# Kernel tuning notes

Measured on AMD Instinct MI355X. Metric: run time of the kernel, lower is better.

## Reference

```python
import jax, jax.numpy as jnp
import numpy as np

NEG_SLOPE = 0.2  # leaky_relu slope used by standard GAT attention


def _gat_layer(h, src, dst, W, a_src, a_dst, gru, n_nodes):
    """One gated multi-head GAT layer.
    h: [N, Din]; W: [H, Din, D]; a_src/a_dst: [H, D]; gru: None or (Wih,Whh,bih,bhh).
    Heads are merged by mean so output is [N, D].
    """
    Wh = jnp.einsum('nd,hdo->nho', h, W)                      # [N, H, D]
    es = jnp.einsum('nho,ho->nh', Wh, a_src)                  # [N, H]
    ed = jnp.einsum('nho,ho->nh', Wh, a_dst)                  # [N, H]
    e = jax.nn.leaky_relu(es[src] + ed[dst], NEG_SLOPE)       # [E, H]
    # edge softmax over each destination's in-neighborhood (segment softmax)
    m = jax.ops.segment_max(e, dst, num_segments=n_nodes)     # [N, H]
    w = jnp.exp(e - m[dst])                                   # [E, H]
    denom = jax.ops.segment_sum(w, dst, num_segments=n_nodes) # [N, H]
    alpha = w / denom[dst]                                    # [E, H]
    # gather-source / scatter-add aggregation
    agg = jax.ops.segment_sum(alpha[:, :, None] * Wh[src], dst,
                              num_segments=n_nodes)           # [N, H, D]
    out = jax.nn.elu(agg.mean(axis=1))                        # [N, D] (head-mean merge)
    if gru is not None:
        Wih, Whh, bih, bhh = gru
        gi = out @ Wih.T + bih                                # [N, 3D]
        gh = h @ Whh.T + bhh                                  # [N, 3D]
        ir, iz, in_ = jnp.split(gi, 3, axis=-1)
        hr, hz, hn = jnp.split(gh, 3, axis=-1)
        r = jax.nn.sigmoid(ir + hr)
        z = jax.nn.sigmoid(iz + hz)
        n = jnp.tanh(in_ + r * hn)
        out = (1.0 - z) * n + z * h                           # GRU-gated residual update
    return out


def setup_inputs() -> dict:
    N, E, D, H, OUT = 20000, 320000, 128, 4, 1
    key = jax.random.key(0)
    ks = jax.random.split(key, 24)
    sd = 1.0 / np.sqrt(D)
    inp = {
        'h': jax.random.normal(ks[0], (N, D), jnp.float32),
        'edge_index': jax.random.randint(ks[1], (2, E), 0, N, jnp.int64),
    }
    # GAT layers: layer1-3 have H heads, layer4 has 1 head
    heads = [H, H, H, 1]
    for i, hh in enumerate(heads, start=1):
        inp[f'W{i}'] = jax.random.normal(ks[2 + 3 * i], (hh, D, D), jnp.float32) * sd
        inp[f'as{i}'] = jax.random.normal(ks[3 + 3 * i], (hh, D), jnp.float32) * 0.1
        inp[f'ad{i}'] = jax.random.normal(ks[4 + 3 * i], (hh, D), jnp.float32) * 0.1
    # shared GRUSubLayer(hidden_dim) parameters (torch GRUCell layout)
    inp['Wih'] = jax.random.normal(ks[18], (3 * D, D), jnp.float32) * sd
    inp['Whh'] = jax.random.normal(ks[19], (3 * D, D), jnp.float32) * sd
    inp['bih'] = jnp.zeros((3 * D,), jnp.float32)
    inp['bhh'] = jnp.zeros((3 * D,), jnp.float32)
    # output head
    inp['W5'] = jax.random.normal(ks[20], (D, OUT), jnp.float32) * sd
    inp['b5'] = jnp.zeros((OUT,), jnp.float32)
    return inp


def reference(h, edge_index, W1, as1, ad1, W2, as2, ad2, W3, as3, ad3,
              W4, as4, ad4, Wih, Whh, bih, bhh, W5, b5):
    N = h.shape[0]
    src, dst = edge_index[0], edge_index[1]
    gru = (Wih, Whh, bih, bhh)
    h = _gat_layer(h, src, dst, W1, as1, ad1, None, N)   # require_gru=False
    h = _gat_layer(h, src, dst, W2, as2, ad2, gru, N)
    h = _gat_layer(h, src, dst, W3, as3, ad3, gru, N)
    h = _gat_layer(h, src, dst, W4, as4, ad4, gru, N)    # single head
    return jax.nn.sigmoid(h @ W5 + b5)                   # [N, out_dim]
```

## Files before the change

kernel.cpp:

```cpp
#include <hip/hip_runtime.h>
#include <math.h>

#define D 128

typedef __attribute__((ext_vector_type(8))) short bf16x8;
typedef __attribute__((ext_vector_type(4))) float f32x4;
typedef __attribute__((ext_vector_type(2))) float f32x2;

__device__ __forceinline__ float sigmoidf_(float x) { return 1.f / (1.f + __expf(-x)); }
__device__ __forceinline__ float bf2f(unsigned short u) { return __uint_as_float(((unsigned)u) << 16); }
__device__ __forceinline__ float u2f_lo(unsigned u) { return __uint_as_float(u << 16); }
__device__ __forceinline__ float u2f_hi(unsigned u) { return __uint_as_float(u & 0xffff0000u); }
__device__ __forceinline__ unsigned short f2b(float f) {
  unsigned u = __float_as_uint(f);
  return (unsigned short)((u + 0x7fffu + ((u >> 16) & 1u)) >> 16);
}
__device__ __forceinline__ float leaky_(float v) { return v > 0.f ? v : 0.2f * v; }

__device__ __forceinline__ void pack_post_elem(const float* __restrict__ W,
                                               unsigned short* __restrict__ Bp, int i, float scale) {
  int j = i & 7;
  int lane = (i >> 3) & 63;
  int rest = i >> 9;
  int db = rest & 7;
  int kb = rest >> 3;
  int k = kb * 32 + ((lane >> 4) << 3) + j;
  int d = db * 16 + (lane & 15);
  int h = k >> 7, kk = k & 127;
  Bp[i] = f2b(W[((size_t)h * 128 + kk) * 128 + d] * scale);
}
__device__ __forceinline__ void pack_gru_elem(const float* __restrict__ S,
                                              unsigned short* __restrict__ Bp, int i) {
  int j = i & 7;
  int lane = (i >> 3) & 63;
  int rest = i >> 9;
  int db = rest % 24;
  int kb = rest / 24;
  int k = kb * 32 + ((lane >> 4) << 3) + j;
  int col = db * 16 + (lane & 15);
  Bp[i] = f2b(S[(size_t)col * 128 + k]);
}

__global__ void __launch_bounds__(256) k_prep(const float* __restrict__ h0, unsigned short* __restrict__ h0b,
// ... 107 lines not shown
  if ((int)blockIdx.x < nS) {
    int e = blockIdx.x * 256 + threadIdx.x;
    if (e < E) {
      int pos = atomicAdd(&fill[dst[e]], 1);
      srcs[pos] = src[e];
    }
    return;
  }
  const int blk = blockIdx.x - nS;
  const int w = threadIdx.x >> 6;
  const int lane = threadIdx.x & 63;
  const int r = lane & 15, g = lane >> 4;
  const int n0 = blk * 64 + w * 16;
  f32x4 acc = (f32x4)0.f;
  const int koff = g << 3;
#pragma unroll
  for (int kb = 0; kb < 4; ++kb) {
    int row = min(n0 + r, N - 1);
    bf16x8 a = *(const bf16x8*)&hb[(size_t)row * 128 + kb * 32 + koff];
    bf16x8 b = *(const bf16x8*)&Pp[((size_t)(kb * 64) + lane) * 8];
    acc = __builtin_amdgcn_mfma_f32_16x16x32_bf16(a, b, acc, 0, 0, 0);
  }
  const int rbase = n0 + g * 4;
#pragma unroll
  for (int i = 0; i < 4; ++i) {
    int row = rbase + i;
    if (row < N) {
      if (r < 4) es[(size_t)row * 4 + r] = acc[i];
      else if (r < 8) ed[(size_t)row * 4 + (r - 4)] = acc[i];
    }
  }
}

template <int H>
__global__ void __launch_bounds__(256) k_edge_gather(const int* __restrict__ rowptr,
                                                     const int* __restrict__ srcs,
                                                     const float* __restrict__ es,
                                                     const float* __restrict__ ed,
                                                     const unsigned short* __restrict__ hb,
                                                     unsigned short* __restrict__ tb, int N) {
  __shared__ __align__(16) unsigned s_off[8][32];
  __shared__ __align__(16) float s_af[8][32][H == 1 ? 1 : 4];
  const int slot = threadIdx.x >> 5;
  const int t = blockIdx.x * 8 + slot;
  if (t >= N) return;
  const int l = threadIdx.x & 31;
  const int q = l & 15;
  const int eg = l >> 4;
  const int b0 = rowptr[t];
  const int deg = rowptr[t + 1] - b0;
  unsigned short* trow = tb + (size_t)t * (H * 128);
  if (deg == 0) {
    if (l < 16) {
#pragma unroll
      for (int h = 0; h < H; ++h)
        *(uint4*)&trow[h * 128 + q * 8] = make_uint4(0u, 0u, 0u, 0u);
    }
    return;
  }
  float edv[H];
#pragma unroll
  for (int h = 0; h < H; ++h) edv[h] = ed[(size_t)t * H + h];

  f32x2 acc[H][4];
#pragma unroll
  for (int h = 0; h < H; ++h)
#pragma unroll
    for (int j = 0; j < 4; ++j) acc[h][j] = (f32x2)0.f;
  const char* hbase = (const char*)hb + q * 16;

  if (deg <= 32) {
    const bool act = l < deg;
    int s = 0;
    float vv[H];
    if (act) {
      s = srcs[b0 + l];
      if constexpr (H == 4) {
        float4 ev = *(const float4*)&es[(size_t)s * 4];
        vv[0] = leaky_(ev.x + edv[0]);
        vv[1] = leaky_(ev.y + edv[1]);
        vv[2] = leaky_(ev.z + edv[2]);
        vv[3] = leaky_(ev.w + edv[3]);
      } else {
        vv[0] = leaky_(es[s] + edv[0]);
      }
    } else {
#pragma unroll
      for (int h = 0; h < H; ++h) vv[h] = -1e30f;
    }
    float mv[H];
#pragma unroll
    for (int h = 0; h < H; ++h) mv[h] = vv[h];
#pragma unroll
    for (int off = 16; off; off >>= 1)
#pragma unroll
      for (int h = 0; h < H; ++h) mv[h] = fmaxf(mv[h], __shfl_xor(mv[h], off));
    float e[H], den[H];
#pragma unroll
    for (int h = 0; h < H; ++h) {
      e[h] = act ? __expf(vv[h] - mv[h]) : 0.f;
      den[h] = e[h];
    }
#pragma unroll
    for (int off = 16; off; off >>= 1)
#pragma unroll
      for (int h = 0; h < H; ++h) den[h] += __shfl_xor(den[h], off);
    s_off[slot][l] = act ? ((unsigned)s << 8) : 0u;
#pragma unroll
    for (int h = 0; h < H; ++h) s_af[slot][l][h] = e[h] * (1.f / den[h]);
    const int steps = (deg + 1) >> 1;
#pragma unroll 4
    for (int e2 = 0; e2 < steps; ++e2) {
      const int ei = e2 * 2 + eg;
      unsigned off = s_off[slot][ei];
      float af[H];
      if constexpr (H == 4) {
        float4 a4 = *(const float4*)&s_af[slot][ei][0];
        af[0] = a4.x; af[1] = a4.y; af[2] = a4.z; af[3] = a4.w;
      } else {
        af[0] = s_af[slot][ei][0];
      }
      uint4 v = *(const uint4*)(hbase + off);
      f32x2 vf0 = {u2f_lo(v.x), u2f_hi(v.x)};
      f32x2 vf1 = {u2f_lo(v.y), u2f_hi(v.y)};
      f32x2 vf2 = {u2f_lo(v.z), u2f_hi(v.z)};
      f32x2 vf3 = {u2f_lo(v.w), u2f_hi(v.w)};
#pragma unroll
      for (int h = 0; h < H; ++h) {
        f32x2 a2 = {af[h], af[h]};
        acc[h][0] += a2 * vf0;
        acc[h][1] += a2 * vf1;
        acc[h][2] += a2 * vf2;
        acc[h][3] += a2 * vf3;
      }
    }
  } else {
    float m[H], den[H], vreg[H];
    int sreg = 0;
#pragma unroll
    for (int h = 0; h < H; ++h) {
      m[h] = -1e30f;
      den[h] = 0.f;
      vreg[h] = -1e30f;
    }
    for (int i = l; i < deg; i += 32) {
      int s = srcs[b0 + i];
      float vv[H];
      if constexpr (H == 4) {
        float4 ev = *(const float4*)&es[(size_t)s * 4];
        vv[0] = ev.x + edv[0];
        vv[1] = ev.y + edv[1];
        vv[2] = ev.z + edv[2];
        vv[3] = ev.w + edv[3];
      } else {
        vv[0] = es[s] + edv[0];
      }
#pragma unroll
      for (int h = 0; h < H; ++h) {
        float v = leaky_(vv[h]);
        vv[h] = v;
        float nm = fmaxf(m[h], v);
        den[h] = den[h] * __expf(m[h] - nm) + __expf(v - nm);
        m[h] = nm;
      }
      if (i == l) {
        sreg = s;
#pragma unroll
        for (int h = 0; h < H; ++h) vreg[h] = vv[h];
      }
    }
#pragma unroll
    for (int off = 16; off; off >>= 1) {
#pragma unroll
      for (int h = 0; h < H; ++h) {
        float om = __shfl_xor(m[h], off);
        float od = __shfl_xor(den[h], off);
        float nm = fmaxf(m[h], om);
        den[h] = den[h] * __expf(m[h] - nm) + od * __expf(om - nm);
        m[h] = nm;
      }
    }
    float rden[H];
#pragma unroll
    for (int h = 0; h < H; ++h) rden[h] = 1.f / den[h];
    for (int c0 = 0; c0 < deg; c0 += 32) {
      const int ce = min(32, deg - c0);
      if (c0 == 0) {
        bool ok = l < deg;
        s_off[slot][l] = ok ? ((unsigned)sreg << 8) : 0u;
#pragma unroll
        for (int h = 0; h < H; ++h)
          s_af[slot][l][h] = ok ? (__expf(vreg[h] - m[h]) * rden[h]) : 0.f;
      } else {
        int i = c0 + l;
        bool ok = i < deg;
        int s = ok ? srcs[b0 + i] : 0;
        s_off[slot][l] = ok ? ((unsigned)s << 8) : 0u;
        float af[H];
#pragma unroll
        for (int h = 0; h < H; ++h) af[h] = 0.f;
        if (ok) {
          float vv[H];
          if constexpr (H == 4) {
            float4 ev = *(const float4*)&es[(size_t)s * 4];
            vv[0] = ev.x + edv[0];
            vv[1] = ev.y + edv[1];
            vv[2] = ev.z + edv[2];
            vv[3] = ev.w + edv[3];
          } else {
            vv[0] = es[s] + edv[0];
          }
#pragma unroll
          for (int h = 0; h < H; ++h)
            af[h] = __expf(leaky_(vv[h]) - m[h]) * rden[h];
        }
#pragma unroll
        for (int h = 0; h < H; ++h) s_af[slot][l][h] = af[h];
      }
      const int steps = (ce + 1) >> 1;
#pragma unroll 4
      for (int e2 = 0; e2 < steps; ++e2) {
        const int ei = e2 * 2 + eg;
        unsigned off = s_off[slot][ei];
        float af[H];
        if constexpr (H == 4) {
          float4 a4 = *(const float4*)&s_af[slot][ei][0];
          af[0] = a4.x; af[1] = a4.y; af[2] = a4.z; af[3] = a4.w;
        } else {
          af[0] = s_af[slot][ei][0];
        }
        uint4 v = *(const uint4*)(hbase + off);
        f32x2 vf0 = {u2f_lo(v.x), u2f_hi(v.x)};
        f32x2 vf1 = {u2f_lo(v.y), u2f_hi(v.y)};
        f32x2 vf2 = {u2f_lo(v.z), u2f_hi(v.z)};
        f32x2 vf3 = {u2f_lo(v.w), u2f_hi(v.w)};
#pragma unroll
        for (int h = 0; h < H; ++h) {
          f32x2 a2 = {af[h], af[h]};
          acc[h][0] += a2 * vf0;
          acc[h][1] += a2 * vf1;
          acc[h][2] += a2 * vf2;
          acc[h][3] += a2 * vf3;
        }
      }
    }
  }
#pragma unroll
  for (int h = 0; h < H; ++h)
#pragma unroll
    for (int j = 0; j < 4; ++j) {
      acc[h][j].x += __shfl_xor(acc[h][j].x, 16);
      acc[h][j].y += __shfl_xor(acc[h][j].y, 16);
    }
  if (l < 16) {
#pragma unroll
    for (int h = 0; h < H; ++h) {
      uint4 pk;
      pk.x = (unsigned)f2b(acc[h][0].x) | ((unsigned)f2b(acc[h][0].y) << 16);
      pk.y = (unsigned)f2b(acc[h][1].x) | ((unsigned)f2b(acc[h][1].y) << 16);
      pk.z = (unsigned)f2b(acc[h][2].x) | ((unsigned)f2b(acc[h][2].y) << 16);
      pk.w = (unsigned)f2b(acc[h][3].x) | ((unsigned)f2b(acc[h][3].y) << 16);
      *(uint4*)&trow[h * 128 + q * 8] = pk;
    }
  }
}

__global__ void __launch_bounds__(256) k_post1(const unsigned short* __restrict__ tb,
                                               const unsigned short* __restrict__ Bp,
                                               float* __restrict__ houtf,
                                               unsigned short* __restrict__ houtb,
                                               const float* __restrict__ Pf,
                                               float* __restrict__ es, float* __restrict__ ed) {
  __shared__ float s_pr[16][8][4];
  const int n0 = blockIdx.x * 16;
  const int w = threadIdx.x >> 6;
  const int lane = threadIdx.x & 63;
  const int r = lane & 15, g = lane >> 4;
  f32x4 acc[2];
  acc[0] = (f32x4)0.f;
  acc[1] = (f32x4)0.f;
  const int koff = g << 3;
#pragma unroll
  for (int kb = 0; kb < 16; ++kb) {
    bf16x8 a = *(const bf16x8*)&tb[(size_t)(n0 + r) * 512 + kb * 32 + koff];
#pragma unroll
    for (int t = 0; t < 2; ++t) {
      bf16x8 b = *(const bf16x8*)&Bp[((size_t)(kb * 8 + w * 2 + t) * 64 + lane) * 8];
      acc[t] = __builtin_amdgcn_mfma_f32_16x16x32_bf16(a, b, acc[t], 0, 0, 0);
    }
  }
  float ps[4][8];
#pragma unroll
  for (int i = 0; i < 4; ++i)
#pragma unroll
    for (int c = 0; c < 8; ++c) ps[i][c] = 0.f;
#pragma unroll
  for (int t = 0; t < 2; ++t) {
    const int col = (w * 2 + t) * 16 + r;
    float4 pj0 = *(const float4*)&Pf[col * 8];
    float4 pj1 = *(const float4*)&Pf[col * 8 + 4];
#pragma unroll
    for (int i = 0; i < 4; ++i) {
      const int row = n0 + g * 4 + i;
      float o = acc[t][i];
      o = o > 0.f ? o : expm1f(o);
      houtf[(size_t)row * 128 + col] = o;
      houtb[(size_t)row * 128 + col] = f2b(o);
      ps[i][0] += o * pj0.x; ps[i][1] += o * pj0.y;
      ps[i][2] += o * pj0.z; ps[i][3] += o * pj0.w;
      ps[i][4] += o * pj1.x; ps[i][5] += o * pj1.y;
      ps[i][6] += o * pj1.z; ps[i][7] += o * pj1.w;
    }
  }
#pragma unroll
  for (int off = 1; off < 16; off <<= 1)
#pragma unroll
    for (int i = 0; i < 4; ++i)
#pragma unroll
      for (int c = 0; c < 8; ++c) ps[i][c] += __shfl_xor(ps[i][c], off);
  if (r == 0) {
#pragma unroll
    for (int i = 0; i < 4; ++i)
#pragma unroll
      for (int c = 0; c < 8; ++c) s_pr[g * 4 + i][c][w] = ps[i][c];
  }
  __syncthreads();
  if (threadIdx.x < 128) {
    int row = threadIdx.x >> 3;
    int c = threadIdx.x & 7;
    float val = s_pr[row][c][0] + s_pr[row][c][1] + s_pr[row][c][2] + s_pr[row][c][3];
    int gr = n0 + row;
    if (c < 4) es[(size_t)gr * 4 + c] = val;
    else ed[(size_t)gr * 4 + (c - 4)] = val;
  }
}

template <int KD, int MODE>
__global__ void __launch_bounds__(256) k_postgru(const unsigned short* __restrict__ tb,
                                                 const unsigned short* __restrict__ Bp,
                                                 const unsigned short* __restrict__ hb,
                                                 const float* __restrict__ hf,
                                                 const unsigned short* __restrict__ Bih,
                                                 const unsigned short* __restrict__ Bhh,
                                                 const float* __restrict__ bih,
                                                 const float* __restrict__ bhh,
                                                 float* __restrict__ houtf,
                                                 unsigned short* __restrict__ houtb,
                                                 const float* __restrict__ Pf,
                                                 float* __restrict__ es, float* __restrict__ ed, int Hn,
                                                 const float* __restrict__ W5,
                                                 const float* __restrict__ b5,
                                                 float* __restrict__ out) {
  __shared__ unsigned short xs[16][136];
  __shared__ float s_pr[16][8][4];
  const int n0 = blockIdx.x * 16;
  const int w = threadIdx.x >> 6;
  const int lane = threadIdx.x & 63;
  const int r = lane & 15, g = lane >> 4;
  const int koff = g << 3;
  {
    f32x4 acc[2];
    acc[0] = (f32x4)0.f;
    acc[1] = (f32x4)0.f;
#pragma unroll
    for (int kb = 0; kb < KD / 32; ++kb) {
      bf16x8 a = *(const bf16x8*)&tb[(size_t)(n0 + r) * KD + kb * 32 + koff];
#pragma unroll
      for (int t = 0; t < 2; ++t) {
        bf16x8 b = *(const bf16x8*)&Bp[((size_t)(kb * 8 + w * 2 + t) * 64 + lane) * 8];
        acc[t] = __builtin_amdgcn_mfma_f32_16x16x32_bf16(a, b, acc[t], 0, 0, 0);
      }
    }
#pragma unroll
    for (int t = 0; t < 2; ++t) {
      const int col = (w * 2 + t) * 16 + r;
#pragma unroll
      for (int i = 0; i < 4; ++i) {
        float o = acc[t][i];
        o = o > 0.f ? o : expm1f(o);
        xs[g * 4 + i][col] = f2b(o);
      }
    }
  }
  __syncthreads();
  const int qbase = w * 2;
  f32x4 ai[3][2], ah[3][2];
#pragma unroll
  for (int p = 0; p < 3; ++p)
#pragma unroll
    for (int t = 0; t < 2; ++t) {
      ai[p][t] = (f32x4)0.f;
      ah[p][t] = (f32x4)0.f;
    }
#pragma unroll
  for (int kb = 0; kb < 4; ++kb) {
    bf16x8 ax = *(const bf16x8*)&xs[r][kb * 32 + koff];
    bf16x8 ahr = *(const bf16x8*)&hb[(size_t)(n0 + r) * 128 + kb * 32 + koff];
#pragma unroll
    for (int p = 0; p < 3; ++p) {
#pragma unroll
      for (int t = 0; t < 2; ++t) {
        const int ct = p * 8 + qbase + t;
        bf16x8 bi = *(const bf16x8*)&Bih[((size_t)(kb * 24 + ct) * 64 + lane) * 8];
        bf16x8 bh = *(const bf16x8*)&Bhh[((size_t)(kb * 24 + ct) * 64 + lane) * 8];
        ai[p][t] = __builtin_amdgcn_mfma_f32_16x16x32_bf16(ax, bi, ai[p][t], 0, 0, 0);
        ah[p][t] = __builtin_amdgcn_mfma_f32_16x16x32_bf16(ahr, bh, ah[p][t], 0, 0, 0);
      }
    }
  }
  if constexpr (MODE == 0) {
    float ps[4][8];
#pragma unroll
    for (int i = 0; i < 4; ++i)
#pragma unroll
      for (int c = 0; c < 8; ++c) ps[i][c] = 0.f;
#pragma unroll
    for (int t = 0; t < 2; ++t) {
      const int j = (qbase + t) * 16 + r;
      const float bir = bih[j], biz = bih[128 + j], bin = bih[256 + j];
      const float bhr = bhh[j], bhz = bhh[128 + j], bhn = bhh[256 + j];
      float4 pj0 = *(const float4*)&Pf[j * 8];
      float4 pj1 = *(const float4*)&Pf[j * 8 + 4];
#pragma unroll
      for (int i = 0; i < 4; ++i) {
        const int row = n0 + g * 4 + i;
        float rr = sigmoidf_(ai[0][t][i] + bir + ah[0][t][i] + bhr);
        float z = sigmoidf_(ai[1][t][i] + biz + ah[1][t][i] + bhz);
        float nn = tanhf(ai[2][t][i] + bin + rr * (ah[2][t][i] + bhn));
        float hp = hf[(size_t)row * 128 + j];
        float o = (1.f - z) * nn + z * hp;
        houtf[(size_t)row * 128 + j] = o;
        houtb[(size_t)row * 128 + j] = f2b(o);
        ps[i][0] += o * pj0.x; ps[i][1] += o * pj0.y;
        ps[i][2] += o * pj0.z; ps[i][3] += o * pj0.w;
        ps[i][4] += o * pj1.x; ps[i][5] += o * pj1.y;
        ps[i][6] += o * pj1.z; ps[i][7] += o * pj1.w;
      }
    }
#pragma unroll
    for (int off = 1; off < 16; off <<= 1)
#pragma unroll
      for (int i = 0; i < 4; ++i)
#pragma unroll
        for (int c = 0; c < 8; ++c) ps[i][c] += __shfl_xor(ps[i][c], off);
    if (r == 0) {
#pragma unroll
      for (int i = 0; i < 4; ++i)
#pragma unroll
        for (int c = 0; c < 8; ++c) s_pr[g * 4 + i][c][w] = ps[i][c];
    }
    __syncthreads();
    if (threadIdx.x < 128) {
      int row = threadIdx.x >> 3;
      int c = threadIdx.x & 7;
      float val = s_pr[row][c][0] + s_pr[row][c][1] + s_pr[row][c][2] + s_pr[row][c][3];
      int gr = n0 + row;
      if (c < Hn) es[(size_t)gr * Hn + c] = val;
      else if (c >= 4 && c < 4 + Hn) ed[(size_t)gr * Hn + (c - 4)] = val;
    }
  } else {
    float pfin[4] = {0.f, 0.f, 0.f, 0.f};
#pragma unroll
    for (int t = 0; t < 2; ++t) {
      const int j = (qbase + t) * 16 + r;
      const float bir = bih[j], biz = bih[128 + j], bin = bih[256 + j];
      const float bhr = bhh[j], bhz = bhh[128 + j], bhn = bhh[256 + j];
      const float w5 = W5[j];
#pragma unroll
      for (int i = 0; i < 4; ++i) {
        const int row = n0 + g * 4 + i;
        float rr = sigmoidf_(ai[0][t][i] + bir + ah[0][t][i] + bhr);
        float z = sigmoidf_(ai[1][t][i] + biz + ah[1][t][i] + bhz);
        float nn = tanhf(ai[2][t][i] + bin + rr * (ah[2][t][i] + bhn));
        float hp = hf[(size_t)row * 128 + j];
        float o = (1.f - z) * nn + z * hp;
        pfin[i] += o * w5;
      }
    }
#pragma unroll
    for (int off = 1; off < 16; off <<= 1)
#pragma unroll
      for (int i = 0; i < 4; ++i) pfin[i] += __shfl_xor(pfin[i], off);
    if (r == 0) {
#pragma unroll
      for (int i = 0; i < 4; ++i) s_pr[g * 4 + i][0][w] = pfin[i];
    }
    __syncthreads();
    if (threadIdx.x < 16) {
      float s = s_pr[threadIdx.x][0][0] + s_pr[threadIdx.x][0][1] +
                s_pr[threadIdx.x][0][2] + s_pr[threadIdx.x][0][3] + b5[0];
      out[n0 + threadIdx.x] = sigmoidf_(s);
    }
  }
}

extern "C" void kernel_launch(void* const* d_in, const int* in_sizes, int n_in,
                              void* d_out, int out_size, void* d_ws, size_t ws_size,
                              hipStream_t stream) {
  const float* h0 = (const float*)d_in[0];
  const int* ei = (const int*)d_in[1];
  const float* W1 = (const float*)d_in[2];
  const float* as1 = (const float*)d_in[3];
  const float* ad1 = (const float*)d_in[4];
  const float* W2 = (const float*)d_in[5];
  const float* as2 = (const float*)d_in[6];
  const float* ad2 = (const float*)d_in[7];
  const float* W3 = (const float*)d_in[8];
  const float* as3 = (const float*)d_in[9];
  const float* ad3 = (const float*)d_in[10];
  const float* W4 = (const float*)d_in[11];
  const float* as4 = (const float*)d_in[12];
  const float* ad4 = (const float*)d_in[13];
  const float* Wih = (const float*)d_in[14];
  const float* Whh = (const float*)d_in[15];
  const float* bih = (const float*)d_in[16];
  const float* bhh = (const float*)d_in[17];
  const float* W5 = (const float*)d_in[18];
  const float* b5 = (const float*)d_in[19];

  const int N = in_sizes[0] / D;
  const int E = in_sizes[1] / 2;
  const int* src = ei;
  const int* dst = ei + E;

  float* ws = (float*)d_ws;
  unsigned short* tb = (unsigned short*)ws;
  float* hA = ws + (size_t)N * 256;
  float* hB = hA + (size_t)N * 128;
  float* es = hB + (size_t)N * 128;
  float* ed = es + (size_t)N * 4;
  unsigned short* h0b = (unsigned short*)(ed + (size_t)N * 4);
  unsigned short* hAb = h0b + (size_t)N * 128;
  unsigned short* hBb = hAb + (size_t)N * 128;
  unsigned short* B1 = hBb + (size_t)N * 128;
  unsigned short* B2 = B1 + 65536;
  unsigned short* B3 = B2 + 65536;
  unsigned short* B4 = B3 + 65536;
  unsigned short* Bih = B4 + 16384;
  unsigned short* Bhh = Bih + 49152;
  unsigned short* Pp1 = Bhh + 49152;
  float* Pf2 = (float*)(Pp1 + 2048);
  float* Pf3 = Pf2 + 1024;
  float* Pf4 = Pf3 + 1024;
  int* deg = (int*)(Pf4 + 1024);
  int* rowptr = deg + N;
  int* fill = rowptr + N + 1;
  int* srcs = fill + N;

  hipMemsetAsync(deg, 0, (size_t)N * 4, stream);
  {
    const int total = N * 128 + 311296 + 2048 + 3072 + E;
    k_prep<<<(total + 255) / 256, 256, 0, stream>>>(
        h0, h0b, W1, W2, W3, W4, Wih, Whh, B1, B2, B3, B4, Bih, Bhh,
        as1, ad1, as2, ad2, as3, ad3, as4, ad4, Pp1, Pf2, Pf3, Pf4, dst, deg, N, E);
  }
  k_scan<<<1, 1024, 0, stream>>>(deg, rowptr, fill, N);
  {
    const int nS = (E + 255) / 256;
    const int nE = (N + 63) / 64;
    k_scatter_esed<<<nS + nE, 256, 0, stream>>>(src, dst, fill, srcs, E,
                                                h0b, Pp1, es, ed, N, nS);
  }

  const int gE = (N + 7) / 8;
  const int gP = N / 16;

  k_edge_gather<4><<<gE, 256, 0, stream>>>(rowptr, srcs, es, ed, h0b, tb, N);
  k_post1<<<gP, 256, 0, stream>>>(tb, B1, hA, hAb, Pf2, es, ed);
  k_edge_gather<4><<<gE, 256, 0, stream>>>(rowptr, srcs, es, ed, hAb, tb, N);
  k_postgru<512, 0><<<gP, 256, 0, stream>>>(tb, B2, hAb, hA, Bih, Bhh, bih, bhh, hB, hBb,
                                            Pf3, es, ed, 4, nullptr, nullptr, nullptr);
  k_edge_gather<4><<<gE, 256, 0, stream>>>(rowptr, srcs, es, ed, hBb, tb, N);
  k_postgru<512, 0><<<gP, 256, 0, stream>>>(tb, B3, hBb, hB, Bih, Bhh, bih, bhh, hA, hAb,
                                            Pf4, es, ed, 1, nullptr, nullptr, nullptr);
  k_edge_gather<1><<<gE, 256, 0, stream>>>(rowptr, srcs, es, ed, hAb, tb, N);
  k_postgru<128, 1><<<gP, 256, 0, stream>>>(tb, B4, hAb, hA, Bih, Bhh, bih, bhh,
                                            nullptr, nullptr, nullptr, nullptr, nullptr, 0,
                                            W5, b5, (float*)d_out);
}
```

Baseline: 267.0 us.

## Fuse edge gather with post-projection/GRU into one kernel per layer

Merges the per-layer edge softmax/gather kernel and the following projection+GRU kernel into a single 512-thread kernel that keeps the aggregated 16-row tile in shared memory instead of writing it to a global bf16 buffer. It also double-buffers the es/ed attention logits so one layer's writes do not race with reads by other blocks of the same launch. This removes the global round-trip of the aggregation buffer and halves the launch count, at the cost of much larger shared memory per block (lower occupancy) and serialising the gather and MFMA phases within a block.

```diff
diff --git a/kernel.cpp b/kernel.cpp
--- a/kernel.cpp
+++ b/kernel.cpp
@@ -8,7 +8,6 @@
 typedef __attribute__((ext_vector_type(2))) float f32x2;
 
 __device__ __forceinline__ float sigmoidf_(float x) { return 1.f / (1.f + __expf(-x)); }
-__device__ __forceinline__ float bf2f(unsigned short u) { return __uint_as_float(((unsigned)u) << 16); }
 __device__ __forceinline__ float u2f_lo(unsigned u) { return __uint_as_float(u << 16); }
 __device__ __forceinline__ float u2f_hi(unsigned u) { return __uint_as_float(u & 0xffff0000u); }
 __device__ __forceinline__ unsigned short f2b(float f) {
@@ -182,174 +181,136 @@
   }
 }
 
-template <int H>
-__global__ void __launch_bounds__(256) k_edge_gather(const int* __restrict__ rowptr,
-                                                     const int* __restrict__ srcs,
-                                                     const float* __restrict__ es,
-                                                     const float* __restrict__ ed,
-                                                     const unsigned short* __restrict__ hb,
-                                                     unsigned short* __restrict__ tb, int N) {
-  __shared__ __align__(16) unsigned s_off[8][32];
-  __shared__ __align__(16) float s_af[8][32][H == 1 ? 1 : 4];
-  const int slot = threadIdx.x >> 5;
-  const int t = blockIdx.x * 8 + slot;
-  if (t >= N) return;
-  const int l = threadIdx.x & 31;
-  const int q = l & 15;
-  const int eg = l >> 4;
-  const int b0 = rowptr[t];
-  const int deg = rowptr[t + 1] - b0;
-  unsigned short* trow = tb + (size_t)t * (H * 128);
-  if (deg == 0) {
-    if (l < 16) {
+template <int H, int MODE>
+__global__ void __launch_bounds__(512) k_layer(const int* __restrict__ rowptr,
+                                               const int* __restrict__ srcs,
+                                               const float* __restrict__ es,
+                                               const float* __restrict__ ed,
+                                               const unsigned short* __restrict__ hbG,
+                                               const unsigned short* __restrict__ Bp,
+                                               const float* __restrict__ hf,
+                                               const unsigned short* __restrict__ Bih,
+                                               const unsigned short* __restrict__ Bhh,
+                                               const float* __restrict__ bih,
+                                               const float* __restrict__ bhh,
+                                               float* __restrict__ houtf,
+                                               unsigned short* __restrict__ houtb,
+                                               const float* __restrict__ Pf,
+                                               float* __restrict__ eso, float* __restrict__ edo, int Hn,
+                                               const float* __restrict__ W5,
+                                               const float* __restrict__ b5,
+                                               float* __restrict__ out) {
+  constexpr int KD = H * 128;
+  __shared__ unsigned short ts[16][KD + 8];
+  __shared__ unsigned short xs[16][136];
+  __shared__ float s_pr[16][8][8];
+  __shared__ __align__(16) unsigned s_off[16][32];
+  __shared__ __align__(16) float s_af[16][32][H == 1 ? 1 : 4];
+
+  const int tid = threadIdx.x;
+  const int n0 = blockIdx.x * 16;
+
+  {
+    const int slot = tid >> 5;
+    const int t = n0 + slot;
+    const int l = tid & 31;
+    const int q = l & 15;
+    const int eg = l >> 4;
+    const int b0 = rowptr[t];
+    const int deg = rowptr[t + 1] - b0;
+    if (deg == 0) {
+      if (l < 16) {
+#pragma unroll
+        for (int h = 0; h < H; ++h)
+          *(uint4*)&ts[slot][h * 128 + q * 8] = make_uint4(0u, 0u, 0u, 0u);
+      }
+    } else {
+      float edv[H];
+#pragma unroll
+      for (int h = 0; h < H; ++h) edv[h] = ed[(size_t)t * H + h];
+      f32x2 acc[H][4];
 #pragma unroll
       for (int h = 0; h < H; ++h)
-        *(uint4*)&trow[h * 128 + q * 8] = make_uint4(0u, 0u, 0u, 0u);
-    }
-    return;
-  }
-  float edv[H];
-#pragma unroll
-  for (int h = 0; h < H; ++h) edv[h] = ed[(size_t)t * H + h];
-
-  f32x2 acc[H][4];
-#pragma unroll
-  for (int h = 0; h < H; ++h)
-#pragma unroll
-    for (int j = 0; j < 4; ++j) acc[h][j] = (f32x2)0.f;
-  const char* hbase = (const char*)hb + q * 16;
-
-  if (deg <= 32) {
-    const bool act = l < deg;
-    int s = 0;
-    float vv[H];
-    if (act) {
-      s = srcs[b0 + l];
-      if constexpr (H == 4) {
-        float4 ev = *(const float4*)&es[(size_t)s * 4];
-        vv[0] = leaky_(ev.x + edv[0]);
-        vv[1] = leaky_(ev.y + edv[1]);
-        vv[2] = leaky_(ev.z + edv[2]);
-        vv[3] = leaky_(ev.w + edv[3]);
+#pragma unroll
+        for (int j = 0; j < 4; ++j) acc[h][j] = (f32x2)0.f;
+      const char* hbase = (const char*)hbG + q * 16;
+
+      if (deg <= 32) {
+        const bool act = l < deg;
+        int s = 0;
+        float vv[H];
+        if (act) {
+          s = srcs[b0 + l];
+          if constexpr (H == 4) {
+            float4 ev = *(const float4*)&es[(size_t)s * 4];
+            vv[0] = leaky_(ev.x + edv[0]);
+            vv[1] = leaky_(ev.y + edv[1]);
+            vv[2] = leaky_(ev.z + edv[2]);
+            vv[3] = leaky_(ev.w + edv[3]);
+          } else {
+            vv[0] = leaky_(es[s] + edv[0]);
+          }
+        } else {
+#pragma unroll
+          for (int h = 0; h < H; ++h) vv[h] = -1e30f;
+        }
+        float mv[H];
+#pragma unroll
+        for (int h = 0; h < H; ++h) mv[h] = vv[h];
+#pragma unroll
+        for (int off = 16; off; off >>= 1)
+#pragma unroll
+          for (int h = 0; h < H; ++h) mv[h] = fmaxf(mv[h], __shfl_xor(mv[h], off));
+        float e[H], den[H];
+#pragma unroll
+        for (int h = 0; h < H; ++h) {
+          e[h] = act ? __expf(vv[h] - mv[h]) : 0.f;
+          den[h] = e[h];
+        }
+#pragma unroll
+        for (int off = 16; off; off >>= 1)
+#pragma unroll
+          for (int h = 0; h < H; ++h) den[h] += __shfl_xor(den[h], off);
+        s_off[slot][l] = act ? ((unsigned)s << 8) : 0u;
+#pragma unroll
+        for (int h = 0; h < H; ++h) s_af[slot][l][h] = e[h] * (1.f / den[h]);
+        const int steps = (deg + 1) >> 1;
+#pragma unroll 4
+        for (int e2 = 0; e2 < steps; ++e2) {
+          const int ei = e2 * 2 + eg;
+          unsigned off = s_off[slot][ei];
+          float af[H];
+          if constexpr (H == 4) {
+            float4 a4 = *(const float4*)&s_af[slot][ei][0];
+            af[0] = a4.x; af[1] = a4.y; af[2] = a4.z; af[3] = a4.w;
+          } else {
+            af[0] = s_af[slot][ei][0];
+          }
+          uint4 v = *(const uint4*)(hbase + off);
+          f32x2 vf0 = {u2f_lo(v.x), u2f_hi(v.x)};
+          f32x2 vf1 = {u2f_lo(v.y), u2f_hi(v.y)};
+          f32x2 vf2 = {u2f_lo(v.z), u2f_hi(v.z)};
+          f32x2 vf3 = {u2f_lo(v.w), u2f_hi(v.w)};
+#pragma unroll
+          for (int h = 0; h < H; ++h) {
+            f32x2 a2 = {af[h], af[h]};
+            acc[h][0] += a2 * vf0;
+            acc[h][1] += a2 * vf1;
+            acc[h][2] += a2 * vf2;
+            acc[h][3] += a2 * vf3;
+          }
+        }
       } else {
-        vv[0] = leaky_(es[s] + edv[0]);
-      }
-    } else {
-#pragma unroll
-      for (int h = 0; h < H; ++h) vv[h] = -1e30f;
-    }
-    float mv[H];
-#pragma unroll
-    for (int h = 0; h < H; ++h) mv[h] = vv[h];
-#pragma unroll
-    for (int off = 16; off; off >>= 1)
-#pragma unroll
-      for (int h = 0; h < H; ++h) mv[h] = fmaxf(mv[h], __shfl_xor(mv[h], off));
-    float e[H], den[H];
-#pragma unroll
-    for (int h = 0; h < H; ++h) {
-      e[h] = act ? __expf(vv[h] - mv[h]) : 0.f;
-      den[h] = e[h];
-    }
-#pragma unroll
-    for (int off = 16; off; off >>= 1)
-#pragma unroll
-      for (int h = 0; h < H; ++h) den[h] += __shfl_xor(den[h], off);
-    s_off[slot][l] = act ? ((unsigned)s << 8) : 0u;
-#pragma unroll
-    for (int h = 0; h < H; ++h) s_af[slot][l][h] = e[h] * (1.f / den[h]);
-    const int steps = (deg + 1) >> 1;
-#pragma unroll 4
-    for (int e2 = 0; e2 < steps; ++e2) {
-      const int ei = e2 * 2 + eg;
-      unsigned off = s_off[slot][ei];
-      float af[H];
-      if constexpr (H == 4) {
-        float4 a4 = *(const float4*)&s_af[slot][ei][0];
-        af[0] = a4.x; af[1] = a4.y; af[2] = a4.z; af[3] = a4.w;
-      } else {
-        af[0] = s_af[slot][ei][0];
-      }
-      uint4 v = *(const uint4*)(hbase + off);
-      f32x2 vf0 = {u2f_lo(v.x), u2f_hi(v.x)};
-      f32x2 vf1 = {u2f_lo(v.y), u2f_hi(v.y)};
-      f32x2 vf2 = {u2f_lo(v.z), u2f_hi(v.z)};
-      f32x2 vf3 = {u2f_lo(v.w), u2f_hi(v.w)};
-#pragma unroll
-      for (int h = 0; h < H; ++h) {
-        f32x2 a2 = {af[h], af[h]};
-        acc[h][0] += a2 * vf0;
-        acc[h][1] += a2 * vf1;
-        acc[h][2] += a2 * vf2;
-        acc[h][3] += a2 * vf3;
-      }
-    }
-  } else {
-    float m[H], den[H], vreg[H];
-    int sreg = 0;
-#pragma unroll
-    for (int h = 0; h < H; ++h) {
-      m[h] = -1e30f;
-      den[h] = 0.f;
-      vreg[h] = -1e30f;
-    }
-    for (int i = l; i < deg; i += 32) {
-      int s = srcs[b0 + i];
-      float vv[H];
-      if constexpr (H == 4) {
-        float4 ev = *(const float4*)&es[(size_t)s * 4];
-        vv[0] = ev.x + edv[0];
-        vv[1] = ev.y + edv[1];
-        vv[2] = ev.z + edv[2];
-        vv[3] = ev.w + edv[3];
-      } else {
-        vv[0] = es[s] + edv[0];
-      }
-#pragma unroll
-      for (int h = 0; h < H; ++h) {
-        float v = leaky_(vv[h]);
-        vv[h] = v;
-        float nm = fmaxf(m[h], v);
-        den[h] = den[h] * __expf(m[h] - nm) + __expf(v - nm);
-        m[h] = nm;
-      }
-      if (i == l) {
-        sreg = s;
-#pragma unroll
-        for (int h = 0; h < H; ++h) vreg[h] = vv[h];
-      }
-    }
-#pragma unroll
-    for (int off = 16; off; off >>= 1) {
-#pragma unroll
-      for (int h = 0; h < H; ++h) {
-        float om = __shfl_xor(m[h], off);
-        float od = __shfl_xor(den[h], off);
-        float nm = fmaxf(m[h], om);
-        den[h] = den[h] * __expf(m[h] - nm) + od * __expf(om - nm);
-        m[h] = nm;
-      }
-    }
-    float rden[H];
-#pragma unroll
-    for (int h = 0; h < H; ++h) rden[h] = 1.f / den[h];
-    for (int c0 = 0; c0 < deg; c0 += 32) {
-      const int ce = min(32, deg - c0);
-      if (c0 == 0) {
-        bool ok = l < deg;
-        s_off[slot][l] = ok ? ((unsigned)sreg << 8) : 0u;
-#pragma unroll
-        for (int h = 0; h < H; ++h)
-          s_af[slot][l][h] = ok ? (__expf(vreg[h] - m[h]) * rden[h]) : 0.f;
-      } else {
-        int i = c0 + l;
-        bool ok = i < deg;
-        int s = ok ? srcs[b0 + i] : 0;
-        s_off[slot][l] = ok ? ((unsigned)s << 8) : 0u;
-        float af[H];
-#pragma unroll
-        for (int h = 0; h < H; ++h) af[h] = 0.f;
-        if (ok) {
+        float m[H], den[H], vreg[H];
+        int sreg = 0;
+#pragma unroll
+        for (int h = 0; h < H; ++h) {
+          m[h] = -1e30f;
+          den[h] = 0.f;
+          vreg[h] = -1e30f;
+        }
+        for (int i = l; i < deg; i += 32) {
+          int s = srcs[b0 + i];
           float vv[H];
           if constexpr (H == 4) {
             float4 ev = *(const float4*)&es[(size_t)s * 4];
@@ -361,98 +322,142 @@
             vv[0] = es[s] + edv[0];
           }
 #pragma unroll
-          for (int h = 0; h < H; ++h)
-            af[h] = __expf(leaky_(vv[h]) - m[h]) * rden[h];
-        }
-#pragma unroll
-        for (int h = 0; h < H; ++h) s_af[slot][l][h] = af[h];
-      }
-      const int steps = (ce + 1) >> 1;
+          for (int h = 0; h < H; ++h) {
+            float v = leaky_(vv[h]);
+            vv[h] = v;
+            float nm = fmaxf(m[h], v);
+            den[h] = den[h] * __expf(m[h] - nm) + __expf(v - nm);
+            m[h] = nm;
+          }
+          if (i == l) {
+            sreg = s;
+#pragma unroll
+            for (int h = 0; h < H; ++h) vreg[h] = vv[h];
+          }
+        }
+#pragma unroll
+        for (int off = 16; off; off >>= 1) {
+#pragma unroll
+          for (int h = 0; h < H; ++h) {
+            float om = __shfl_xor(m[h], off);
+            float od = __shfl_xor(den[h], off);
+            float nm = fmaxf(m[h], om);
+            den[h] = den[h] * __expf(m[h] - nm) + od * __expf(om - nm);
+            m[h] = nm;
+          }
+        }
+        float rden[H];
+#pragma unroll
+        for (int h = 0; h < H; ++h) rden[h] = 1.f / den[h];
+        for (int c0 = 0; c0 < deg; c0 += 32) {
+          const int ce = min(32, deg - c0);
+          if (c0 == 0) {
+            bool ok = l < deg;
+            s_off[slot][l] = ok ? ((unsigned)sreg << 8) : 0u;
+#pragma unroll
+            for (int h = 0; h < H; ++h)
+              s_af[slot][l][h] = ok ? (__expf(vreg[h] - m[h]) * rden[h]) : 0.f;
+          } else {
+            int i = c0 + l;
+            bool ok = i < deg;
+            int s = ok ? srcs[b0 + i] : 0;
+            s_off[slot][l] = ok ? ((unsigned)s << 8) : 0u;
+            float af[H];
+#pragma unroll
+            for (int h = 0; h < H; ++h) af[h] = 0.f;
+            if (ok) {
+              float vv[H];
+              if constexpr (H == 4) {
+                float4 ev = *(const float4*)&es[(size_t)s * 4];
+                vv[0] = ev.x + edv[0];
+                vv[1] = ev.y + edv[1];
+                vv[2] = ev.z + edv[2];
+                vv[3] = ev.w + edv[3];
+              } else {
+                vv[0] = es[s] + edv[0];
+              }
+#pragma unroll
+              for (int h = 0; h < H; ++h)
+                af[h] = __expf(leaky_(vv[h]) - m[h]) * rden[h];
+            }
+#pragma unroll
+            for (int h = 0; h < H; ++h) s_af[slot][l][h] = af[h];
+          }
+          const int steps = (ce + 1) >> 1;
 #pragma unroll 4
-      for (int e2 = 0; e2 < steps; ++e2) {
-        const int ei = e2 * 2 + eg;
-        unsigned off = s_off[slot][ei];
-        float af[H];
-        if constexpr (H == 4) {
-          float4 a4 = *(const float4*)&s_af[slot][ei][0];
-          af[0] = a4.x; af[1] = a4.y; af[2] = a4.z; af[3] = a4.w;
-        } else {
-          af[0] = s_af[slot][ei][0];
-        }
-        uint4 v = *(const uint4*)(hbase + off);
-        f32x2 vf0 = {u2f_lo(v.x), u2f_hi(v.x)};
-        f32x2 vf1 = {u2f_lo(v.y), u2f_hi(v.y)};
-        f32x2 vf2 = {u2f_lo(v.z), u2f_hi(v.z)};
-        f32x2 vf3 = {u2f_lo(v.w), u2f_hi(v.w)};
+          for (int e2 = 0; e2 < steps; ++e2) {
+            const int ei = e2 * 2 + eg;
+            unsigned off = s_off[slot][ei];
+            float af[H];
+            if constexpr (H == 4) {
+              float4 a4 = *(const float4*)&s_af[slot][ei][0];
+              af[0] = a4.x; af[1] = a4.y; af[2] = a4.z; af[3] = a4.w;
+            } else {
+              af[0] = s_af[slot][ei][0];
+            }
+            uint4 v = *(const uint4*)(hbase + off);
+            f32x2 vf0 = {u2f_lo(v.x), u2f_hi(v.x)};
+            f32x2 vf1 = {u2f_lo(v.y), u2f_hi(v.y)};
+            f32x2 vf2 = {u2f_lo(v.z), u2f_hi(v.z)};
+            f32x2 vf3 = {u2f_lo(v.w), u2f_hi(v.w)};
+#pragma unroll
+            for (int h = 0; h < H; ++h) {
+              f32x2 a2 = {af[h], af[h]};
+              acc[h][0] += a2 * vf0;
+              acc[h][1] += a2 * vf1;
+              acc[h][2] += a2 * vf2;
+              acc[h][3] += a2 * vf3;
+            }
+          }
+        }
+      }
+#pragma unroll
+      for (int h = 0; h < H; ++h)
+#pragma unroll
+        for (int j = 0; j < 4; ++j) {
+          acc[h][j].x += __shfl_xor(acc[h][j].x, 16);
+          acc[h][j].y += __shfl_xor(acc[h][j].y, 16);
+        }
+      if (l < 16) {
 #pragma unroll
         for (int h = 0; h < H; ++h) {
-          f32x2 a2 = {af[h], af[h]};
-          acc[h][0] += a2 * vf0;
-          acc[h][1] += a2 * vf1;
-          acc[h][2] += a2 * vf2;
-          acc[h][3] += a2 * vf3;
-        }
-      }
-    }
-  }
-#pragma unroll
-  for (int h = 0; h < H; ++h)
-#pragma unroll
-    for (int j = 0; j < 4; ++j) {
-      acc[h][j].x += __shfl_xor(acc[h][j].x, 16);
-      acc[h][j].y += __shfl_xor(acc[h][j].y, 16);
-    }
-  if (l < 16) {
-#pragma unroll
-    for (int h = 0; h < H; ++h) {
-      uint4 pk;
-      pk.x = (unsigned)f2b(acc[h][0].x) | ((unsigned)f2b(acc[h][0].y) << 16);
-      pk.y = (unsigned)f2b(acc[h][1].x) | ((unsigned)f2b(acc[h][1].y) << 16);
-      pk.z = (unsigned)f2b(acc[h][2].x) | ((unsigned)f2b(acc[h][2].y) << 16);
-      pk.w = (unsigned)f2b(acc[h][3].x) | ((unsigned)f2b(acc[h][3].y) << 16);
-      *(uint4*)&trow[h * 128 + q * 8] = pk;
-    }
-  }
-}
-
-__global__ void __launch_bounds__(256) k_post1(const unsigned short* __restrict__ tb,
-                                               const unsigned short* __restrict__ Bp,
-                                               float* __restrict__ houtf,
-                                               unsigned short* __restrict__ houtb,
-                                               const float* __restrict__ Pf,
-                                               float* __restrict__ es, float* __restrict__ ed) {
-  __shared__ float s_pr[16][8][4];
-  const int n0 = blockIdx.x * 16;
-  const int w = threadIdx.x >> 6;
-  const int lane = threadIdx.x & 63;
+          uint4 pk;
+          pk.x = (unsigned)f2b(acc[h][0].x) | ((unsigned)f2b(acc[h][0].y) << 16);
+          pk.y = (unsigned)f2b(acc[h][1].x) | ((unsigned)f2b(acc[h][1].y) << 16);
+          pk.z = (unsigned)f2b(acc[h][2].x) | ((unsigned)f2b(acc[h][2].y) << 16);
+          pk.w = (unsigned)f2b(acc[h][3].x) | ((unsigned)f2b(acc[h][3].y) << 16);
+          *(uint4*)&ts[slot][h * 128 + q * 8] = pk;
+        }
+      }
+    }
+  }
+  __syncthreads();
+
+  const int w = tid >> 6;
+  const int lane = tid & 63;
   const int r = lane & 15, g = lane >> 4;
-  f32x4 acc[2];
-  acc[0] = (f32x4)0.f;
-  acc[1] = (f32x4)0.f;
   const int koff = g << 3;
-#pragma unroll
-  for (int kb = 0; kb < 16; ++kb) {
-    bf16x8 a = *(const bf16x8*)&tb[(size_t)(n0 + r) * 512 + kb * 32 + koff];
-#pragma unroll
-    for (int t = 0; t < 2; ++t) {
-      bf16x8 b = *(const bf16x8*)&Bp[((size_t)(kb * 8 + w * 2 + t) * 64 + lane) * 8];
-      acc[t] = __builtin_amdgcn_mfma_f32_16x16x32_bf16(a, b, acc[t], 0, 0, 0);
-    }
-  }
-  float ps[4][8];
-#pragma unroll
-  for (int i = 0; i < 4; ++i)
-#pragma unroll
-    for (int c = 0; c < 8; ++c) ps[i][c] = 0.f;
-#pragma unroll
-  for (int t = 0; t < 2; ++t) {
-    const int col = (w * 2 + t) * 16 + r;
+  f32x4 pacc = (f32x4)0.f;
+#pragma unroll
+  for (int kb = 0; kb < KD / 32; ++kb) {
+    bf16x8 a = *(const bf16x8*)&ts[r][kb * 32 + koff];
+    bf16x8 b = *(const bf16x8*)&Bp[((size_t)(kb * 8 + w) * 64 + lane) * 8];
+    pacc = __builtin_amdgcn_mfma_f32_16x16x32_bf16(a, b, pacc, 0, 0, 0);
+  }
+  const int col = w * 16 + r;
+
+  if constexpr (MODE == 0) {
+    float ps[4][8];
+#pragma unroll
+    for (int i = 0; i < 4; ++i)
+#pragma unroll
+      for (int c = 0; c < 8; ++c) ps[i][c] = 0.f;
     float4 pj0 = *(const float4*)&Pf[col * 8];
     float4 pj1 = *(const float4*)&Pf[col * 8 + 4];
 #pragma unroll
     for (int i = 0; i < 4; ++i) {
       const int row = n0 + g * 4 + i;
-      float o = acc[t][i];
+      float o = pacc[i];
       o = o > 0.f ? o : expm1f(o);
       houtf[(size_t)row * 128 + col] = o;
       houtb[(size_t)row * 128 + col] = f2b(o);
@@ -461,122 +466,73 @@
       ps[i][4] += o * pj1.x; ps[i][5] += o * pj1.y;
       ps[i][6] += o * pj1.z; ps[i][7] += o * pj1.w;
     }
-  }
-#pragma unroll
-  for (int off = 1; off < 16; off <<= 1)
-#pragma unroll
-    for (int i = 0; i < 4; ++i)
-#pragma unroll
-      for (int c = 0; c < 8; ++c) ps[i][c] += __shfl_xor(ps[i][c], off);
-  if (r == 0) {
-#pragma unroll
-    for (int i = 0; i < 4; ++i)
-#pragma unroll
-      for (int c = 0; c < 8; ++c) s_pr[g * 4 + i][c][w] = ps[i][c];
-  }
-  __syncthreads();
-  if (threadIdx.x < 128) {
-    int row = threadIdx.x >> 3;
-    int c = threadIdx.x & 7;
-    float val = s_pr[row][c][0] + s_pr[row][c][1] + s_pr[row][c][2] + s_pr[row][c][3];
-    int gr = n0 + row;
-    if (c < 4) es[(size_t)gr * 4 + c] = val;
-    else ed[(size_t)gr * 4 + (c - 4)] = val;
-  }
-}
-
-template <int KD, int MODE>
-__global__ void __launch_bounds__(256) k_postgru(const unsigned short* __restrict__ tb,
-                                                 const unsigned short* __restrict__ Bp,
-                                                 const unsigned short* __restrict__ hb,
-                                                 const float* __restrict__ hf,
-                                                 const unsigned short* __restrict__ Bih,
-                                                 const unsigned short* __restrict__ Bhh,
-                                                 const float* __restrict__ bih,
-                                                 const float* __restrict__ bhh,
-                                                 float* __restrict__ houtf,
-                                                 unsigned short* __restrict__ houtb,
-                                                 const float* __restrict__ Pf,
-                                                 float* __restrict__ es, float* __restrict__ ed, int Hn,
-                                                 const float* __restrict__ W5,
-                                                 const float* __restrict__ b5,
-                                                 float* __restrict__ out) {
-  __shared__ unsigned short xs[16][136];
-  __shared__ float s_pr[16][8][4];
-  const int n0 = blockIdx.x * 16;
-  const int w = threadIdx.x >> 6;
-  const int lane = threadIdx.x & 63;
-  const int r = lane & 15, g = lane >> 4;
-  const int koff = g << 3;
-  {
-    f32x4 acc[2];
-    acc[0] = (f32x4)0.f;
-    acc[1] = (f32x4)0.f;
-#pragma unroll
-    for (int kb = 0; kb < KD / 32; ++kb) {
-      bf16x8 a = *(const bf16x8*)&tb[(size_t)(n0 + r) * KD + kb * 32 + koff];
-#pragma unroll
-      for (int t = 0; t < 2; ++t) {
-        bf16x8 b = *(const bf16x8*)&Bp[((size_t)(kb * 8 + w * 2 + t) * 64 + lane) * 8];
-        acc[t] = __builtin_amdgcn_mfma_f32_16x16x32_bf16(a, b, acc[t], 0, 0, 0);
-      }
-    }
-#pragma unroll
-    for (int t = 0; t < 2; ++t) {
-      const int col = (w * 2 + t) * 16 + r;
-#pragma unroll
-      for (int i = 0; i < 4; ++i) {
-        float o = acc[t][i];
-        o = o > 0.f ? o : expm1f(o);
-        xs[g * 4 + i][col] = f2b(o);
-      }
-    }
-  }
-  __syncthreads();
-  const int qbase = w * 2;
-  f32x4 ai[3][2], ah[3][2];
-#pragma unroll
-  for (int p = 0; p < 3; ++p)
-#pragma unroll
-    for (int t = 0; t < 2; ++t) {
-      ai[p][t] = (f32x4)0.f;
-      ah[p][t] = (f32x4)0.f;
-    }
-#pragma unroll
-  for (int kb = 0; kb < 4; ++kb) {
-    bf16x8 ax = *(const bf16x8*)&xs[r][kb * 32 + koff];
-    bf16x8 ahr = *(const bf16x8*)&hb[(size_t)(n0 + r) * 128 + kb * 32 + koff];
+#pragma unroll
+    for (int off = 1; off < 16; off <<= 1)
+#pragma unroll
+      for (int i = 0; i < 4; ++i)
+#pragma unroll
+        for (int c = 0; c < 8; ++c) ps[i][c] += __shfl_xor(ps[i][c], off);
+    if (r == 0) {
+#pragma unroll
+      for (int i = 0; i < 4; ++i)
+#pragma unroll
+        for (int c = 0; c < 8; ++c) s_pr[g * 4 + i][c][w] = ps[i][c];
+    }
+    __syncthreads();
+    if (tid < 128) {
+      int row = tid >> 3;
+      int c = tid & 7;
+      float val = 0.f;
+#pragma unroll
+      for (int ww = 0; ww < 8; ++ww) val += s_pr[row][c][ww];
+      int gr = n0 + row;
+      if (c < 4) eso[(size_t)gr * 4 + c] = val;
+      else edo[(size_t)gr * 4 + (c - 4)] = val;
+    }
+  } else {
+#pragma unroll
+    for (int i = 0; i < 4; ++i) {
+      float o = pacc[i];
+      o = o > 0.f ? o : expm1f(o);
+      xs[g * 4 + i][col] = f2b(o);
+    }
+    __syncthreads();
+    f32x4 ai[3], ah[3];
 #pragma unroll
     for (int p = 0; p < 3; ++p) {
-#pragma unroll
-      for (int t = 0; t < 2; ++t) {
-        const int ct = p * 8 + qbase + t;
+      ai[p] = (f32x4)0.f;
+      ah[p] = (f32x4)0.f;
+    }
+#pragma unroll
+    for (int kb = 0; kb < 4; ++kb) {
+      bf16x8 ax = *(const bf16x8*)&xs[r][kb * 32 + koff];
+      bf16x8 ahr = *(const bf16x8*)&hbG[(size_t)(n0 + r) * 128 + kb * 32 + koff];
+#pragma unroll
+      for (int p = 0; p < 3; ++p) {
+        const int ct = p * 8 + w;
         bf16x8 bi = *(const bf16x8*)&Bih[((size_t)(kb * 24 + ct) * 64 + lane) * 8];
         bf16x8 bh = *(const bf16x8*)&Bhh[((size_t)(kb * 24 + ct) * 64 + lane) * 8];
-        ai[p][t] = __builtin_amdgcn_mfma_f32_16x16x32_bf16(ax, bi, ai[p][t], 0, 0, 0);
-        ah[p][t] = __builtin_amdgcn_mfma_f32_16x16x32_bf16(ahr, bh, ah[p][t], 0, 0, 0);
-      }
-    }
-  }
-  if constexpr (MODE == 0) {
-    float ps[4][8];
-#pragma unroll
-    for (int i = 0; i < 4; ++i)
-#pragma unroll
-      for (int c = 0; c < 8; ++c) ps[i][c] = 0.f;
-#pragma unroll
-    for (int t = 0; t < 2; ++t) {
-      const int j = (qbase + t) * 16 + r;
-      const float bir = bih[j], biz = bih[128 + j], bin = bih[256 + j];
-      const float bhr = bhh[j], bhz = bhh[128 + j], bhn = bhh[256 + j];
+        ai[p] = __builtin_amdgcn_mfma_f32_16x16x32_bf16(ax, bi, ai[p], 0, 0, 0);
+        ah[p] = __builtin_amdgcn_mfma_f32_16x16x32_bf16(ahr, bh, ah[p], 0, 0, 0);
+      }
+    }
+    const int j = col;
+    const float bir = bih[j], biz = bih[128 + j], bin = bih[256 + j];
+    const float bhr = bhh[j], bhz = bhh[128 + j], bhn = bhh[256 + j];
+    if constexpr (MODE == 1) {
+      float ps[4][8];
+#pragma unroll
+      for (int i = 0; i < 4; ++i)
+#pragma unroll
+        for (int c = 0; c < 8; ++c) ps[i][c] = 0.f;
       float4 pj0 = *(const float4*)&Pf[j * 8];
       float4 pj1 = *(const float4*)&Pf[j * 8 + 4];
 #pragma unroll
       for (int i = 0; i < 4; ++i) {
         const int row = n0 + g * 4 + i;
-        float rr = sigmoidf_(ai[0][t][i] + bir + ah[0][t][i] + bhr);
-        float z = sigmoidf_(ai[1][t][i] + biz + ah[1][t][i] + bhz);
-        float nn = tanhf(ai[2][t][i] + bin + rr * (ah[2][t][i] + bhn));
+        float rr = sigmoidf_(ai[0][i] + bir + ah[0][i] + bhr);
+        float z = sigmoidf_(ai[1][i] + biz + ah[1][i] + bhz);
+        float nn = tanhf(ai[2][i] + bin + rr * (ah[2][i] + bhn));
         float hp = hf[(size_t)row * 128 + j];
         float o = (1.f - z) * nn + z * hp;
         houtf[(size_t)row * 128 + j] = o;
@@ -586,60 +542,57 @@
         ps[i][4] += o * pj1.x; ps[i][5] += o * pj1.y;
         ps[i][6] += o * pj1.z; ps[i][7] += o * pj1.w;
       }
-    }
-#pragma unroll
-    for (int off = 1; off < 16; off <<= 1)
-#pragma unroll
-      for (int i = 0; i < 4; ++i)
-#pragma unroll
-        for (int c = 0; c < 8; ++c) ps[i][c] += __shfl_xor(ps[i][c], off);
-    if (r == 0) {
-#pragma unroll
-      for (int i = 0; i < 4; ++i)
-#pragma unroll
-        for (int c = 0; c < 8; ++c) s_pr[g * 4 + i][c][w] = ps[i][c];
-    }
-    __syncthreads();
-    if (threadIdx.x < 128) {
-      int row = threadIdx.x >> 3;
-      int c = threadIdx.x & 7;
-      float val = s_pr[row][c][0] + s_pr[row][c][1] + s_pr[row][c][2] + s_pr[row][c][3];
-      int gr = n0 + row;
-      if (c < Hn) es[(size_t)gr * Hn + c] = val;
-      else if (c >= 4 && c < 4 + Hn) ed[(size_t)gr * Hn + (c - 4)] = val;
-    }
-  } else {
-    float pfin[4] = {0.f, 0.f, 0.f, 0.f};
-#pragma unroll
-    for (int t = 0; t < 2; ++t) {
-      const int j = (qbase + t) * 16 + r;
-      const float bir = bih[j], biz = bih[128 + j], bin = bih[256 + j];
-      const float bhr = bhh[j], bhz = bhh[128 + j], bhn = bhh[256 + j];
+#pragma unroll
+      for (int off = 1; off < 16; off <<= 1)
+#pragma unroll
+        for (int i = 0; i < 4; ++i)
+#pragma unroll
+          for (int c = 0; c < 8; ++c) ps[i][c] += __shfl_xor(ps[i][c], off);
+      if (r == 0) {
+#pragma unroll
+        for (int i = 0; i < 4; ++i)
+#pragma unroll
+          for (int c = 0; c < 8; ++c) s_pr[g * 4 + i][c][w] = ps[i][c];
+      }
+      __syncthreads();
+      if (tid < 128) {
+        int row = tid >> 3;
+        int c = tid & 7;
+        float val = 0.f;
+#pragma unroll
+        for (int ww = 0; ww < 8; ++ww) val += s_pr[row][c][ww];
+        int gr = n0 + row;
+        if (c < Hn) eso[(size_t)gr * Hn + c] = val;
+        else if (c >= 4 && c < 4 + Hn) edo[(size_t)gr * Hn + (c - 4)] = val;
+      }
+    } else {
+      float pfin[4] = {0.f, 0.f, 0.f, 0.f};
       const float w5 = W5[j];
 #pragma unroll
       for (int i = 0; i < 4; ++i) {
         const int row = n0 + g * 4 + i;
-        float rr = sigmoidf_(ai[0][t][i] + bir + ah[0][t][i] + bhr);
-        float z = sigmoidf_(ai[1][t][i] + biz + ah[1][t][i] + bhz);
-        float nn = tanhf(ai[2][t][i] + bin + rr * (ah[2][t][i] + bhn));
+        float rr = sigmoidf_(ai[0][i] + bir + ah[0][i] + bhr);
+        float z = sigmoidf_(ai[1][i] + biz + ah[1][i] + bhz);
+        float nn = tanhf(ai[2][i] + bin + rr * (ah[2][i] + bhn));
         float hp = hf[(size_t)row * 128 + j];
         float o = (1.f - z) * nn + z * hp;
         pfin[i] += o * w5;
       }
-    }
-#pragma unroll
-    for (int off = 1; off < 16; off <<= 1)
-#pragma unroll
-      for (int i = 0; i < 4; ++i) pfin[i] += __shfl_xor(pfin[i], off);
-    if (r == 0) {
-#pragma unroll
-      for (int i = 0; i < 4; ++i) s_pr[g * 4 + i][0][w] = pfin[i];
-    }
-    __syncthreads();
-    if (threadIdx.x < 16) {
-      float s = s_pr[threadIdx.x][0][0] + s_pr[threadIdx.x][0][1] +
-                s_pr[threadIdx.x][0][2] + s_pr[threadIdx.x][0][3] + b5[0];
-      out[n0 + threadIdx.x] = sigmoidf_(s);
+#pragma unroll
+      for (int off = 1; off < 16; off <<= 1)
+#pragma unroll
+        for (int i = 0; i < 4; ++i) pfin[i] += __shfl_xor(pfin[i], off);
+      if (r == 0) {
+#pragma unroll
+        for (int i = 0; i < 4; ++i) s_pr[g * 4 + i][0][w] = pfin[i];
+      }
+      __syncthreads();
+      if (tid < 16) {
+        float s = b5[0];
+#pragma unroll
+        for (int ww = 0; ww < 8; ++ww) s += s_pr[tid][0][ww];
+        out[n0 + tid] = sigmoidf_(s);
+      }
     }
   }
 }
@@ -674,12 +627,13 @@
   const int* dst = ei + E;
 
   float* ws = (float*)d_ws;
-  unsigned short* tb = (unsigned short*)ws;
-  float* hA = ws + (size_t)N * 256;
+  float* hA = ws;
   float* hB = hA + (size_t)N * 128;
-  float* es = hB + (size_t)N * 128;
-  float* ed = es + (size_t)N * 4;
-  unsigned short* h0b = (unsigned short*)(ed + (size_t)N * 4);
+  float* esA = hB + (size_t)N * 128;
+  float* edA = esA + (size_t)N * 4;
+  float* esB = edA + (size_t)N * 4;
+  float* edB = esB + (size_t)N * 4;
+  unsigned short* h0b = (unsigned short*)(edB + (size_t)N * 4);
   unsigned short* hAb = h0b + (size_t)N * 128;
   unsigned short* hBb = hAb + (size_t)N * 128;
   unsigned short* B1 = hBb + (size_t)N * 128;
@@ -709,22 +663,22 @@
     const int nS = (E + 255) / 256;
     const int nE = (N + 63) / 64;
     k_scatter_esed<<<nS + nE, 256, 0, stream>>>(src, dst, fill, srcs, E,
-                                                h0b, Pp1, es, ed, N, nS);
-  }
-
-  const int gE = (N + 7) / 8;
-  const int gP = N / 16;
-
-  k_edge_gather<4><<<gE, 256, 0, stream>>>(rowptr, srcs, es, ed, h0b, tb, N);
-  k_post1<<<gP, 256, 0, stream>>>(tb, B1, hA, hAb, Pf2, es, ed);
-  k_edge_gather<4><<<gE, 256, 0, stream>>>(rowptr, srcs, es, ed, hAb, tb, N);
-  k_postgru<512, 0><<<gP, 256, 0, stream>>>(tb, B2, hAb, hA, Bih, Bhh, bih, bhh, hB, hBb,
-                                            Pf3, es, ed, 4, nullptr, nullptr, nullptr);
-  k_edge_gather<4><<<gE, 256, 0, stream>>>(rowptr, srcs, es, ed, hBb, tb, N);
-  k_postgru<512, 0><<<gP, 256, 0, stream>>>(tb, B3, hBb, hB, Bih, Bhh, bih, bhh, hA, hAb,
-                                            Pf4, es, ed, 1, nullptr, nullptr, nullptr);
-  k_edge_gather<1><<<gE, 256, 0, stream>>>(rowptr, srcs, es, ed, hAb, tb, N);
-  k_postgru<128, 1><<<gP, 256, 0, stream>>>(tb, B4, hAb, hA, Bih, Bhh, bih, bhh,
-                                            nullptr, nullptr, nullptr, nullptr, nullptr, 0,
-                                            W5, b5, (float*)d_out);
-}
+                                                h0b, Pp1, esA, edA, N, nS);
+  }
+
+  const int gL = N / 16;
+
+  k_layer<4, 0><<<gL, 512, 0, stream>>>(rowptr, srcs, esA, edA, h0b, B1,
+                                        nullptr, nullptr, nullptr, nullptr, nullptr,
+                                        hA, hAb, Pf2, esB, edB, 4, nullptr, nullptr, nullptr);
+  k_layer<4, 1><<<gL, 512, 0, stream>>>(rowptr, srcs, esB, edB, hAb, B2,
+                                        hA, Bih, Bhh, bih, bhh,
+                                        hB, hBb, Pf3, esA, edA, 4, nullptr, nullptr, nullptr);
+  k_layer<4, 1><<<gL, 512, 0, stream>>>(rowptr, srcs, esA, edA, hBb, B3,
+                                        hB, Bih, Bhh, bih, bhh,
+                                        hA, hAb, Pf4, esB, edB, 1, nullptr, nullptr, nullptr);
+  k_layer<1, 2><<<gL, 512, 0, stream>>>(rowptr, srcs, esB, edB, hAb, B4,
+                                        hA, Bih, Bhh, bih, bhh,
+                                        nullptr, nullptr, nullptr, nullptr, nullptr, 0,
+                                        W5, b5, (float*)d_out);
+}
```

Result: no change. 262.6 us (median of 3 runs) (-1.6%).
